# Kernel optimization log

Hardware: AMD Instinct MI355X
Metric: run time of the kernel (lower is better)

Reference implementation:

```python
import jax, jax.numpy as jnp
import numpy as np

BG_OPACITY = 1e10  # background_opacity
BG_COLOR = 0.0     # bg_color = (0.0,)


def setup_inputs() -> dict:
    key = jax.random.key(0)
    k1, k2, k3, k4 = jax.random.split(key, 4)
    B, R, N, C = 8, 16384, 128, 3
    rays_densities = jax.random.uniform(k1, (B, R, N, 1), dtype=jnp.float32) * 2.0
    rays_features = jax.random.uniform(k2, (B, R, N, C), dtype=jnp.float32)
    # monotonically increasing sample depths along the ray
    steps = jax.random.uniform(k3, (B, R, N), dtype=jnp.float32) * 0.05 + 0.01
    ray_lengths = jnp.cumsum(steps, axis=-1) + 2.0
    ray_directions = jax.random.normal(k4, (B, R, 3), dtype=jnp.float32)
    return {
        "rays_densities": rays_densities,
        "rays_features": rays_features,
        "ray_lengths": ray_lengths,
        "ray_directions": ray_directions,
    }


def reference(rays_densities, rays_features, ray_lengths, ray_directions):
    # deltas between consecutive samples; last delta is the background opacity
    deltas = jnp.concatenate(
        [ray_lengths[..., 1:] - ray_lengths[..., :-1],
         jnp.full_like(ray_lengths[..., :1], BG_OPACITY)], axis=-1)
    dir_norm = jnp.linalg.norm(ray_directions, axis=-1)  # (B, R)
    deltas = deltas * dir_norm[..., None]
    dens = jax.nn.relu(rays_densities[..., 0])  # density_relu=True, bias=0
    weighted = deltas * dens  # (B, R, N)
    capped = 1.0 - jnp.exp(-weighted)  # exponential capping
    rays_opacities = 1.0 - jnp.exp(-jnp.cumsum(weighted, axis=-1))
    opacities = rays_opacities[..., -1:]  # (B, R, 1)
    # roll absorption by surface_thickness=1 and set leading entry to 1
    absorption = 1.0 - rays_opacities
    absorption_shifted = jnp.roll(absorption, 1, axis=-1).at[..., :1].set(1.0)
    weights = capped * absorption_shifted  # product weight function
    depths = jnp.sum(weights * ray_lengths, axis=-1, keepdims=True)
    features = jnp.einsum('brn,brnc->brc', weights, rays_features)
    # blend_output=False -> alpha = 1; bg_color scalar 0.0 broadcast
    features = features + (1.0 - opacities) * BG_COLOR
    return features, depths, opacities, weights
```

## Files before the change

kernel.cpp:

```cpp
#include <hip/hip_runtime.h>


#define BG_OPACITY_F 1e10f

__global__ __launch_bounds__(256) void ea_render_kernel(
    const float* __restrict__ dens,
    const float* __restrict__ feats,
    const float* __restrict__ lens,
    const float* __restrict__ dirs,
    float* __restrict__ out_feat,
    float* __restrict__ out_depth,
    float* __restrict__ out_opac,
    float* __restrict__ out_w,
    int n_rays)
{
    const int wave = threadIdx.x >> 6;
    const int lane = threadIdx.x & 63;
    const long ray = (long)blockIdx.x * 4 + wave;
    if (ray >= n_rays) return;

    const long base = ray * 128;
    const int n0 = lane * 2;

    const float2 d2 = *(const float2*)(dens + base + n0);
    const float2 l2 = *(const float2*)(lens + base + n0);

    const float* dp = dirs + ray * 3;
    const float dx = dp[0], dy = dp[1], dz = dp[2];
    const float dn = sqrtf(dx * dx + dy * dy + dz * dz);

    const float lnext = __shfl_down(l2.x, 1, 64);
    const float delta0 = l2.y - l2.x;
    const float delta1 = (lane == 63) ? BG_OPACITY_F : (lnext - l2.y);

    const float w0 = delta0 * dn * fmaxf(d2.x, 0.0f);
    const float w1 = delta1 * dn * fmaxf(d2.y, 0.0f);

    const float w1s = (lane == 63) ? 0.0f : w1;
    const float s = w0 + w1s;
    float inc = s;
    #pragma unroll
    for (int off = 1; off < 64; off <<= 1) {
        const float t = __shfl_up(inc, off, 64);
        if (lane >= off) inc += t;
    }
    const float excl = inc - s;

    const float e0 = __expf(-w0);
    const float e1 = __expf(-w1);
    const float a0 = __expf(-excl);
    const float a1 = a0 * e0;
    const float wgt0 = (1.0f - e0) * a0;
    const float wgt1 = (1.0f - e1) * a1;

    const float total_real = __shfl(inc, 63, 64);
    const float w1_last    = __shfl(w1, 63, 64);
    const float opac = 1.0f - __expf(-(total_real + w1_last));

    float pd = wgt0 * l2.x + wgt1 * l2.y;

    const float* fp = feats + base * 3 + (long)n0 * 3;
    const float2 f01 = *(const float2*)(fp);
    const float2 f23 = *(const float2*)(fp + 2);
    const float2 f45 = *(const float2*)(fp + 4);
    float fr = wgt0 * f01.x + wgt1 * f23.y;
    float fg = wgt0 * f01.y + wgt1 * f45.x;
    float fb = wgt0 * f23.x + wgt1 * f45.y;

    #pragma unroll
    for (int off = 32; off; off >>= 1) {
        pd += __shfl_xor(pd, off, 64);
        fr += __shfl_xor(fr, off, 64);
        fg += __shfl_xor(fg, off, 64);
        fb += __shfl_xor(fb, off, 64);
    }

    *(float2*)(out_w + base + n0) = make_float2(wgt0, wgt1);

    if (lane == 0) {
        out_feat[ray * 3 + 0] = fr;
        out_feat[ray * 3 + 1] = fg;
        out_feat[ray * 3 + 2] = fb;
        out_depth[ray] = pd;
        out_opac[ray] = opac;
    }
}

extern "C" void kernel_launch(void* const* d_in, const int* in_sizes, int n_in,
                              void* d_out, int out_size, void* d_ws, size_t ws_size,
                              hipStream_t stream) {
    const float* dens  = (const float*)d_in[0];
    const float* feats = (const float*)d_in[1];
    const float* lens  = (const float*)d_in[2];
    const float* dirs  = (const float*)d_in[3];

    const int n_rays = in_sizes[3] / 3;

    float* out = (float*)d_out;
    float* out_feat  = out;
    float* out_depth = out + (long)n_rays * 3;
    float* out_opac  = out + (long)n_rays * 4;
    float* out_w     = out + (long)n_rays * 5;

    const int blocks = (n_rays + 3) / 4;
    ea_render_kernel<<<blocks, 256, 0, stream>>>(
        dens, feats, lens, dirs, out_feat, out_depth, out_opac, out_w, n_rays);
}
```

Baseline: 372.4 us.

## Map 16 lanes per ray with 8 samples per thread and wide loads

Each ray is now handled by 16 lanes instead of a full 64-lane wave, and each thread processes 8 consecutive samples. Loads become 16-byte float4 vectors, the wave scan and reductions shrink from 6 to 4 shuffle steps, and per-sample transmittance is carried serially within a thread. Weight stores use nontemporal 16-byte writes. This cuts shuffle and instruction overhead on a memory-bound kernel, but raises per-thread register use and lowers the number of threads in flight.

```diff
diff --git a/kernel.cpp b/kernel.cpp
--- a/kernel.cpp
+++ b/kernel.cpp
@@ -2,6 +2,8 @@
 
 
 #define BG_OPACITY_F 1e10f
+
+typedef float floatx4 __attribute__((ext_vector_type(4)));
 
 __global__ __launch_bounds__(256) void ea_render_kernel(
     const float* __restrict__ dens,
@@ -14,75 +16,98 @@
     float* __restrict__ out_w,
     int n_rays)
 {
+    const int lane = threadIdx.x & 63;
     const int wave = threadIdx.x >> 6;
-    const int lane = threadIdx.x & 63;
-    const long ray = (long)blockIdx.x * 4 + wave;
+    const int g    = lane >> 4;
+    const int t    = lane & 15;
+    const long ray = (long)blockIdx.x * 16 + wave * 4 + g;
     if (ray >= n_rays) return;
 
     const long base = ray * 128;
-    const int n0 = lane * 2;
+    const int  n0   = t * 8;
 
-    const float2 d2 = *(const float2*)(dens + base + n0);
-    const float2 l2 = *(const float2*)(lens + base + n0);
+    const float4 dA = *(const float4*)(dens + base + n0);
+    const float4 dB = *(const float4*)(dens + base + n0 + 4);
+    const float4 lA = *(const float4*)(lens + base + n0);
+    const float4 lB = *(const float4*)(lens + base + n0 + 4);
+
+    const float* fp = feats + base * 3 + (long)n0 * 3;
+    const float4 f0 = *(const float4*)(fp +  0);
+    const float4 f1 = *(const float4*)(fp +  4);
+    const float4 f2 = *(const float4*)(fp +  8);
+    const float4 f3 = *(const float4*)(fp + 12);
+    const float4 f4 = *(const float4*)(fp + 16);
+    const float4 f5 = *(const float4*)(fp + 20);
 
     const float* dp = dirs + ray * 3;
     const float dx = dp[0], dy = dp[1], dz = dp[2];
     const float dn = sqrtf(dx * dx + dy * dy + dz * dz);
 
-    const float lnext = __shfl_down(l2.x, 1, 64);
-    const float delta0 = l2.y - l2.x;
-    const float delta1 = (lane == 63) ? BG_OPACITY_F : (lnext - l2.y);
+    const float l[8]  = {lA.x, lA.y, lA.z, lA.w, lB.x, lB.y, lB.z, lB.w};
+    const float dv[8] = {dA.x, dA.y, dA.z, dA.w, dB.x, dB.y, dB.z, dB.w};
 
-    const float w0 = delta0 * dn * fmaxf(d2.x, 0.0f);
-    const float w1 = delta1 * dn * fmaxf(d2.y, 0.0f);
+    const float lnext = __shfl_down(lA.x, 1, 64);
 
-    const float w1s = (lane == 63) ? 0.0f : w1;
-    const float s = w0 + w1s;
+    float w[8];
+    #pragma unroll
+    for (int i = 0; i < 7; ++i)
+        w[i] = (l[i + 1] - l[i]) * dn * fmaxf(dv[i], 0.0f);
+    const float delta7 = (t == 15) ? BG_OPACITY_F : (lnext - l[7]);
+    w[7] = delta7 * dn * fmaxf(dv[7], 0.0f);
+    const float w7s = (t == 15) ? 0.0f : w[7];
+
+    const float s = w[0] + w[1] + w[2] + w[3] + w[4] + w[5] + w[6] + w7s;
+
     float inc = s;
     #pragma unroll
-    for (int off = 1; off < 64; off <<= 1) {
-        const float t = __shfl_up(inc, off, 64);
-        if (lane >= off) inc += t;
+    for (int off = 1; off < 16; off <<= 1) {
+        const float u = __shfl_up(inc, off, 64);
+        if (t >= off) inc += u;
     }
     const float excl = inc - s;
 
-    const float e0 = __expf(-w0);
-    const float e1 = __expf(-w1);
-    const float a0 = __expf(-excl);
-    const float a1 = a0 * e0;
-    const float wgt0 = (1.0f - e0) * a0;
-    const float wgt1 = (1.0f - e1) * a1;
+    float a = __expf(-excl);
+    float wgt[8];
+    #pragma unroll
+    for (int i = 0; i < 8; ++i) {
+        const float ei = __expf(-w[i]);
+        wgt[i] = (1.0f - ei) * a;
+        a *= ei;
+    }
 
-    const float total_real = __shfl(inc, 63, 64);
-    const float w1_last    = __shfl(w1, 63, 64);
-    const float opac = 1.0f - __expf(-(total_real + w1_last));
-
-    float pd = wgt0 * l2.x + wgt1 * l2.y;
-
-    const float* fp = feats + base * 3 + (long)n0 * 3;
-    const float2 f01 = *(const float2*)(fp);
-    const float2 f23 = *(const float2*)(fp + 2);
-    const float2 f45 = *(const float2*)(fp + 4);
-    float fr = wgt0 * f01.x + wgt1 * f23.y;
-    float fg = wgt0 * f01.y + wgt1 * f45.x;
-    float fb = wgt0 * f23.x + wgt1 * f45.y;
+    const float f[24] = {f0.x, f0.y, f0.z, f0.w, f1.x, f1.y, f1.z, f1.w,
+                         f2.x, f2.y, f2.z, f2.w, f3.x, f3.y, f3.z, f3.w,
+                         f4.x, f4.y, f4.z, f4.w, f5.x, f5.y, f5.z, f5.w};
+    float pd = 0.0f, fr = 0.0f, fg = 0.0f, fb = 0.0f;
+    #pragma unroll
+    for (int i = 0; i < 8; ++i) {
+        pd += wgt[i] * l[i];
+        fr += wgt[i] * f[3 * i + 0];
+        fg += wgt[i] * f[3 * i + 1];
+        fb += wgt[i] * f[3 * i + 2];
+    }
 
     #pragma unroll
-    for (int off = 32; off; off >>= 1) {
+    for (int off = 8; off; off >>= 1) {
         pd += __shfl_xor(pd, off, 64);
         fr += __shfl_xor(fr, off, 64);
         fg += __shfl_xor(fg, off, 64);
         fb += __shfl_xor(fb, off, 64);
     }
 
-    *(float2*)(out_w + base + n0) = make_float2(wgt0, wgt1);
+    const floatx4 wv0 = {wgt[0], wgt[1], wgt[2], wgt[3]};
+    const floatx4 wv1 = {wgt[4], wgt[5], wgt[6], wgt[7]};
+    __builtin_nontemporal_store(wv0, (floatx4*)(out_w + base + n0));
+    __builtin_nontemporal_store(wv1, (floatx4*)(out_w + base + n0 + 4));
 
-    if (lane == 0) {
+    if (t == 15) {
+        out_opac[ray] = 1.0f - __expf(-(inc + w[7]));
+    }
+    if (t == 0) {
         out_feat[ray * 3 + 0] = fr;
         out_feat[ray * 3 + 1] = fg;
         out_feat[ray * 3 + 2] = fb;
         out_depth[ray] = pd;
-        out_opac[ray] = opac;
     }
 }
 
@@ -102,7 +127,7 @@
     float* out_opac  = out + (long)n_rays * 4;
     float* out_w     = out + (long)n_rays * 5;
 
-    const int blocks = (n_rays + 3) / 4;
+    const int blocks = (n_rays + 15) / 16;
     ea_render_kernel<<<blocks, 256, 0, stream>>>(
         dens, feats, lens, dirs, out_feat, out_depth, out_opac, out_w, n_rays);
 }
```

Result: slower. 380.8 us (+2.2%).

## Process four rays per wavefront with batched loads and nontemporal weight stores

Applied to the files above, without the earlier changes.

Each 64-thread block is now one wavefront that handles four rays. All loads for the four rays are issued up front, which raises memory-level parallelism, and the scans and reductions are interleaved across rays to hide shuffle latency. Weight outputs use nontemporal stores, and opacity is written directly by lane 63 instead of being broadcast. The cost is higher register pressure and smaller blocks, which could reduce occupancy.

```diff
diff --git a/kernel.cpp b/kernel.cpp
--- a/kernel.cpp
+++ b/kernel.cpp
@@ -3,7 +3,9 @@
 
 #define BG_OPACITY_F 1e10f
 
-__global__ __launch_bounds__(256) void ea_render_kernel(
+typedef float floatx2 __attribute__((ext_vector_type(2)));
+
+__global__ __launch_bounds__(64, 4) void ea_render_kernel(
     const float* __restrict__ dens,
     const float* __restrict__ feats,
     const float* __restrict__ lens,
@@ -14,75 +16,118 @@
     float* __restrict__ out_w,
     int n_rays)
 {
-    const int wave = threadIdx.x >> 6;
-    const int lane = threadIdx.x & 63;
-    const long ray = (long)blockIdx.x * 4 + wave;
-    if (ray >= n_rays) return;
-
-    const long base = ray * 128;
+    const int lane = threadIdx.x;
+    const long ray0 = (long)blockIdx.x * 4;
+    if (ray0 >= n_rays) return;
     const int n0 = lane * 2;
 
-    const float2 d2 = *(const float2*)(dens + base + n0);
-    const float2 l2 = *(const float2*)(lens + base + n0);
+    long ray[4];
+    #pragma unroll
+    for (int r = 0; r < 4; ++r) {
+        const long q = ray0 + r;
+        ray[r] = (q < n_rays) ? q : (n_rays - 1);
+    }
 
-    const float* dp = dirs + ray * 3;
-    const float dx = dp[0], dy = dp[1], dz = dp[2];
-    const float dn = sqrtf(dx * dx + dy * dy + dz * dz);
+    float dxv[4], dyv[4], dzv[4];
+    #pragma unroll
+    for (int r = 0; r < 4; ++r) {
+        const float* dp = dirs + ray[r] * 3;
+        dxv[r] = dp[0]; dyv[r] = dp[1]; dzv[r] = dp[2];
+    }
+    float2 d2[4], l2[4];
+    #pragma unroll
+    for (int r = 0; r < 4; ++r) {
+        const long base = ray[r] * 128;
+        d2[r] = *(const float2*)(dens + base + n0);
+        l2[r] = *(const float2*)(lens + base + n0);
+    }
+    float2 f01[4], f23[4], f45[4];
+    #pragma unroll
+    for (int r = 0; r < 4; ++r) {
+        const float* fp = feats + ray[r] * 384 + (long)n0 * 3;
+        f01[r] = *(const float2*)(fp);
+        f23[r] = *(const float2*)(fp + 2);
+        f45[r] = *(const float2*)(fp + 4);
+    }
 
-    const float lnext = __shfl_down(l2.x, 1, 64);
-    const float delta0 = l2.y - l2.x;
-    const float delta1 = (lane == 63) ? BG_OPACITY_F : (lnext - l2.y);
+    float dn[4];
+    #pragma unroll
+    for (int r = 0; r < 4; ++r)
+        dn[r] = sqrtf(dxv[r]*dxv[r] + dyv[r]*dyv[r] + dzv[r]*dzv[r]);
 
-    const float w0 = delta0 * dn * fmaxf(d2.x, 0.0f);
-    const float w1 = delta1 * dn * fmaxf(d2.y, 0.0f);
+    float lnx[4];
+    #pragma unroll
+    for (int r = 0; r < 4; ++r)
+        lnx[r] = __shfl_down(l2[r].x, 1, 64);
 
-    const float w1s = (lane == 63) ? 0.0f : w1;
-    const float s = w0 + w1s;
-    float inc = s;
+    float w0[4], w1[4], s[4];
+    #pragma unroll
+    for (int r = 0; r < 4; ++r) {
+        const float delta0 = l2[r].y - l2[r].x;
+        const float delta1 = (lane == 63) ? BG_OPACITY_F : (lnx[r] - l2[r].y);
+        w0[r] = delta0 * dn[r] * fmaxf(d2[r].x, 0.0f);
+        w1[r] = delta1 * dn[r] * fmaxf(d2[r].y, 0.0f);
+        const float w1s = (lane == 63) ? 0.0f : w1[r];
+        s[r] = w0[r] + w1s;
+    }
+
+    float inc[4];
+    #pragma unroll
+    for (int r = 0; r < 4; ++r) inc[r] = s[r];
     #pragma unroll
     for (int off = 1; off < 64; off <<= 1) {
-        const float t = __shfl_up(inc, off, 64);
-        if (lane >= off) inc += t;
+        #pragma unroll
+        for (int r = 0; r < 4; ++r) {
+            const float t = __shfl_up(inc[r], off, 64);
+            if (lane >= off) inc[r] += t;
+        }
     }
-    const float excl = inc - s;
 
-    const float e0 = __expf(-w0);
-    const float e1 = __expf(-w1);
-    const float a0 = __expf(-excl);
-    const float a1 = a0 * e0;
-    const float wgt0 = (1.0f - e0) * a0;
-    const float wgt1 = (1.0f - e1) * a1;
+    float wgt0[4], wgt1[4];
+    #pragma unroll
+    for (int r = 0; r < 4; ++r) {
+        const float excl = inc[r] - s[r];
+        const float e0 = __expf(-w0[r]);
+        const float e1 = __expf(-w1[r]);
+        const float a0 = __expf(-excl);
+        const float a1 = a0 * e0;
+        wgt0[r] = (1.0f - e0) * a0;
+        wgt1[r] = (1.0f - e1) * a1;
+        const floatx2 wv = {wgt0[r], wgt1[r]};
+        __builtin_nontemporal_store(wv, (floatx2*)(out_w + ray[r] * 128 + n0));
+        if (lane == 63) {
+            out_opac[ray[r]] = 1.0f - __expf(-(inc[r] + w1[r]));
+        }
+    }
 
-    const float total_real = __shfl(inc, 63, 64);
-    const float w1_last    = __shfl(w1, 63, 64);
-    const float opac = 1.0f - __expf(-(total_real + w1_last));
-
-    float pd = wgt0 * l2.x + wgt1 * l2.y;
-
-    const float* fp = feats + base * 3 + (long)n0 * 3;
-    const float2 f01 = *(const float2*)(fp);
-    const float2 f23 = *(const float2*)(fp + 2);
-    const float2 f45 = *(const float2*)(fp + 4);
-    float fr = wgt0 * f01.x + wgt1 * f23.y;
-    float fg = wgt0 * f01.y + wgt1 * f45.x;
-    float fb = wgt0 * f23.x + wgt1 * f45.y;
+    float pd[4], fr[4], fg[4], fb[4];
+    #pragma unroll
+    for (int r = 0; r < 4; ++r) {
+        pd[r] = wgt0[r] * l2[r].x + wgt1[r] * l2[r].y;
+        fr[r] = wgt0[r] * f01[r].x + wgt1[r] * f23[r].y;
+        fg[r] = wgt0[r] * f01[r].y + wgt1[r] * f45[r].x;
+        fb[r] = wgt0[r] * f23[r].x + wgt1[r] * f45[r].y;
+    }
 
     #pragma unroll
     for (int off = 32; off; off >>= 1) {
-        pd += __shfl_xor(pd, off, 64);
-        fr += __shfl_xor(fr, off, 64);
-        fg += __shfl_xor(fg, off, 64);
-        fb += __shfl_xor(fb, off, 64);
+        #pragma unroll
+        for (int r = 0; r < 4; ++r) {
+            pd[r] += __shfl_xor(pd[r], off, 64);
+            fr[r] += __shfl_xor(fr[r], off, 64);
+            fg[r] += __shfl_xor(fg[r], off, 64);
+            fb[r] += __shfl_xor(fb[r], off, 64);
+        }
     }
 
-    *(float2*)(out_w + base + n0) = make_float2(wgt0, wgt1);
-
     if (lane == 0) {
-        out_feat[ray * 3 + 0] = fr;
-        out_feat[ray * 3 + 1] = fg;
-        out_feat[ray * 3 + 2] = fb;
-        out_depth[ray] = pd;
-        out_opac[ray] = opac;
+        #pragma unroll
+        for (int r = 0; r < 4; ++r) {
+            out_feat[ray[r] * 3 + 0] = fr[r];
+            out_feat[ray[r] * 3 + 1] = fg[r];
+            out_feat[ray[r] * 3 + 2] = fb[r];
+            out_depth[ray[r]] = pd[r];
+        }
     }
 }
 
@@ -103,6 +148,6 @@
     float* out_w     = out + (long)n_rays * 5;
 
     const int blocks = (n_rays + 3) / 4;
-    ea_render_kernel<<<blocks, 256, 0, stream>>>(
+    ea_render_kernel<<<blocks, 64, 0, stream>>>(
         dens, feats, lens, dirs, out_feat, out_depth, out_opac, out_w, n_rays);
 }
```

New measurement: 383.2 us. +2.9%, slower.

## Pipeline ray tiles through LDS with async global_load_lds triple buffering

Applied to the files above, without the earlier changes.

The kernel becomes persistent: a grid of at most 2560 single-wave blocks, each looping over two-ray tiles. Density, length and feature data are staged into shared memory with global_load_lds in a three-deep buffer, and each lane now handles 4 samples instead of 2. The weights output uses nontemporal vector stores. The aim is to hide memory latency by prefetching tiles while computing earlier ones, at the cost of hand-written waitcnt synchronisation and reduced occupancy per block.

```diff
diff --git a/kernel.cpp b/kernel.cpp
--- a/kernel.cpp
+++ b/kernel.cpp
@@ -3,7 +3,31 @@
 
 #define BG_OPACITY_F 1e10f
 
-__global__ __launch_bounds__(256) void ea_render_kernel(
+typedef float floatx4 __attribute__((ext_vector_type(4)));
+
+#define BUFW 1280
+#define NBUF 3
+
+__device__ __forceinline__ void stage_tile(const float* __restrict__ dens,
+                                           const float* __restrict__ lens,
+                                           const float* __restrict__ feats,
+                                           float* sbuf, long tile, int lane)
+{
+    typedef const __attribute__((address_space(1))) unsigned int* gp_t;
+    typedef __attribute__((address_space(3))) unsigned int* lp_t;
+    const float* gd = dens + tile * 256 + (long)lane * 4;
+    const float* gl = lens + tile * 256 + (long)lane * 4;
+    __builtin_amdgcn_global_load_lds((gp_t)gd, (lp_t)(sbuf),       16, 0, 0);
+    __builtin_amdgcn_global_load_lds((gp_t)gl, (lp_t)(sbuf + 256), 16, 0, 0);
+    #pragma unroll
+    for (int k = 0; k < 3; ++k) {
+        const float* gf = feats + tile * 768 + (long)(k * 64 + lane) * 4;
+        __builtin_amdgcn_global_load_lds((gp_t)gf,
+                                         (lp_t)(sbuf + 512 + k * 256), 16, 0, 0);
+    }
+}
+
+__global__ __launch_bounds__(64, 2) void ea_render_kernel(
     const float* __restrict__ dens,
     const float* __restrict__ feats,
     const float* __restrict__ lens,
@@ -14,75 +38,114 @@
     float* __restrict__ out_w,
     int n_rays)
 {
-    const int wave = threadIdx.x >> 6;
-    const int lane = threadIdx.x & 63;
-    const long ray = (long)blockIdx.x * 4 + wave;
-    if (ray >= n_rays) return;
+    __shared__ __align__(16) float sm[NBUF * BUFW];
 
-    const long base = ray * 128;
-    const int n0 = lane * 2;
+    const int lane = threadIdx.x;
+    const int t    = lane & 31;
+    const int rb   = lane >> 5;
+    const long NT  = (long)(n_rays + 1) >> 1;
+    const long G   = gridDim.x;
 
-    const float2 d2 = *(const float2*)(dens + base + n0);
-    const float2 l2 = *(const float2*)(lens + base + n0);
+    long tk = blockIdx.x;
+    if (tk >= NT) return;
 
-    const float* dp = dirs + ray * 3;
-    const float dx = dp[0], dy = dp[1], dz = dp[2];
-    const float dn = sqrtf(dx * dx + dy * dy + dz * dz);
+    stage_tile(dens, lens, feats, sm, tk, lane);
+    {
+        long t1 = tk + G; if (t1 >= NT) t1 = NT - 1;
+        stage_tile(dens, lens, feats, sm + BUFW, t1, lane);
+    }
+    long ray0 = tk * 2 + rb; if (ray0 >= n_rays) ray0 = n_rays - 1;
+    float cdx = dirs[ray0 * 3 + 0];
+    float cdy = dirs[ray0 * 3 + 1];
+    float cdz = dirs[ray0 * 3 + 2];
 
-    const float lnext = __shfl_down(l2.x, 1, 64);
-    const float delta0 = l2.y - l2.x;
-    const float delta1 = (lane == 63) ? BG_OPACITY_F : (lnext - l2.y);
+    int bi = 0;
+    for (; tk < NT; tk += G) {
+        long t2 = tk + 2 * G; if (t2 >= NT) t2 = NT - 1;
+        int  b2 = bi + 2; if (b2 >= NBUF) b2 -= NBUF;
+        stage_tile(dens, lens, feats, sm + b2 * BUFW, t2, lane);
 
-    const float w0 = delta0 * dn * fmaxf(d2.x, 0.0f);
-    const float w1 = delta1 * dn * fmaxf(d2.y, 0.0f);
+        asm volatile("s_waitcnt vmcnt(10)" ::: "memory");
+        __builtin_amdgcn_sched_barrier(0);
 
-    const float w1s = (lane == 63) ? 0.0f : w1;
-    const float s = w0 + w1s;
-    float inc = s;
-    #pragma unroll
-    for (int off = 1; off < 64; off <<= 1) {
-        const float t = __shfl_up(inc, off, 64);
-        if (lane >= off) inc += t;
-    }
-    const float excl = inc - s;
+        long tn = tk + G; if (tn >= NT) tn = tk;
+        long rayn = tn * 2 + rb; if (rayn >= n_rays) rayn = n_rays - 1;
+        const float ndx = dirs[rayn * 3 + 0];
+        const float ndy = dirs[rayn * 3 + 1];
+        const float ndz = dirs[rayn * 3 + 2];
 
-    const float e0 = __expf(-w0);
-    const float e1 = __expf(-w1);
-    const float a0 = __expf(-excl);
-    const float a1 = a0 * e0;
-    const float wgt0 = (1.0f - e0) * a0;
-    const float wgt1 = (1.0f - e1) * a1;
+        const float* sc = sm + bi * BUFW;
+        long ray = tk * 2 + rb; if (ray >= n_rays) ray = n_rays - 1;
+        const long base = ray * 128;
+        const int  n0   = t * 4;
 
-    const float total_real = __shfl(inc, 63, 64);
-    const float w1_last    = __shfl(w1, 63, 64);
-    const float opac = 1.0f - __expf(-(total_real + w1_last));
+        const float4 dq = *(const float4*)(sc + lane * 4);
+        const float4 lq = *(const float4*)(sc + 256 + lane * 4);
+        const float* fw = sc + 512 + rb * 384 + t * 12;
+        const float4 q0 = *(const float4*)(fw);
+        const float4 q1 = *(const float4*)(fw + 4);
+        const float4 q2 = *(const float4*)(fw + 8);
 
-    float pd = wgt0 * l2.x + wgt1 * l2.y;
+        const float dn = sqrtf(cdx * cdx + cdy * cdy + cdz * cdz);
 
-    const float* fp = feats + base * 3 + (long)n0 * 3;
-    const float2 f01 = *(const float2*)(fp);
-    const float2 f23 = *(const float2*)(fp + 2);
-    const float2 f45 = *(const float2*)(fp + 4);
-    float fr = wgt0 * f01.x + wgt1 * f23.y;
-    float fg = wgt0 * f01.y + wgt1 * f45.x;
-    float fb = wgt0 * f23.x + wgt1 * f45.y;
+        const float lnext = __shfl_down(lq.x, 1, 64);
 
-    #pragma unroll
-    for (int off = 32; off; off >>= 1) {
-        pd += __shfl_xor(pd, off, 64);
-        fr += __shfl_xor(fr, off, 64);
-        fg += __shfl_xor(fg, off, 64);
-        fb += __shfl_xor(fb, off, 64);
-    }
+        const float w0 = (lq.y - lq.x) * dn * fmaxf(dq.x, 0.0f);
+        const float w1 = (lq.z - lq.y) * dn * fmaxf(dq.y, 0.0f);
+        const float w2 = (lq.w - lq.z) * dn * fmaxf(dq.z, 0.0f);
+        const float delta3 = (t == 31) ? BG_OPACITY_F : (lnext - lq.w);
+        const float w3 = delta3 * dn * fmaxf(dq.w, 0.0f);
+        const float w3s = (t == 31) ? 0.0f : w3;
+        const float s = w0 + w1 + w2 + w3s;
 
-    *(float2*)(out_w + base + n0) = make_float2(wgt0, wgt1);
+        float inc = s;
+        #pragma unroll
+        for (int off = 1; off < 32; off <<= 1) {
+            const float u = __shfl_up(inc, off, 64);
+            if (t >= off) inc += u;
+        }
+        const float excl = inc - s;
 
-    if (lane == 0) {
-        out_feat[ray * 3 + 0] = fr;
-        out_feat[ray * 3 + 1] = fg;
-        out_feat[ray * 3 + 2] = fb;
-        out_depth[ray] = pd;
-        out_opac[ray] = opac;
+        float a = __expf(-excl);
+        const float e0 = __expf(-w0), e1 = __expf(-w1);
+        const float e2 = __expf(-w2), e3 = __expf(-w3);
+        const float g0 = (1.0f - e0) * a;
+        const float a1 = a * e0;
+        const float g1 = (1.0f - e1) * a1;
+        const float a2 = a1 * e1;
+        const float g2 = (1.0f - e2) * a2;
+        const float a3 = a2 * e2;
+        const float g3 = (1.0f - e3) * a3;
+
+        const floatx4 wv = {g0, g1, g2, g3};
+        __builtin_nontemporal_store(wv, (floatx4*)(out_w + base + n0));
+
+        if (t == 31) {
+            out_opac[ray] = 1.0f - __expf(-(inc + w3));
+        }
+
+        float pd = g0 * lq.x + g1 * lq.y + g2 * lq.z + g3 * lq.w;
+        float fr = g0 * q0.x + g1 * q0.w + g2 * q1.z + g3 * q2.y;
+        float fg = g0 * q0.y + g1 * q1.x + g2 * q1.w + g3 * q2.z;
+        float fb = g0 * q0.z + g1 * q1.y + g2 * q2.x + g3 * q2.w;
+
+        #pragma unroll
+        for (int off = 16; off; off >>= 1) {
+            pd += __shfl_xor(pd, off, 64);
+            fr += __shfl_xor(fr, off, 64);
+            fg += __shfl_xor(fg, off, 64);
+            fb += __shfl_xor(fb, off, 64);
+        }
+
+        if (t == 0) {
+            out_feat[ray * 3 + 0] = fr;
+            out_feat[ray * 3 + 1] = fg;
+            out_feat[ray * 3 + 2] = fb;
+            out_depth[ray] = pd;
+        }
+
+        cdx = ndx; cdy = ndy; cdz = ndz;
+        bi += 1; if (bi >= NBUF) bi = 0;
     }
 }
 
@@ -102,7 +165,8 @@
     float* out_opac  = out + (long)n_rays * 4;
     float* out_w     = out + (long)n_rays * 5;
 
-    const int blocks = (n_rays + 3) / 4;
-    ea_render_kernel<<<blocks, 256, 0, stream>>>(
+    const long n_tiles = (long)(n_rays + 1) / 2;
+    const int blocks = (int)(n_tiles < 2560 ? n_tiles : 2560);
+    ea_render_kernel<<<blocks, 64, 0, stream>>>(
         dens, feats, lens, dirs, out_feat, out_depth, out_opac, out_w, n_rays);
 }
```

After: 388.3 us. 4.3% more time.
